# Kernel optimization log

Measured on AMD Instinct MI355X. Metric: run time of the kernel, lower is better.

Reference implementation:

```python
import jax, jax.numpy as jnp
import numpy as np

EMB = 1024
HEAD = 128

def setup_inputs() -> dict:
    key = jax.random.key(0)
    ks = jax.random.split(key, 7)
    B, S = 4, 4096
    x = jax.random.normal(ks[0], (B, S, EMB), dtype=jnp.float32)
    s_in = 1.0 / np.sqrt(EMB)
    Wq = jax.random.uniform(ks[1], (EMB, HEAD), jnp.float32, -s_in, s_in)
    bq = jax.random.uniform(ks[2], (HEAD,), jnp.float32, -s_in, s_in)
    Wk = jax.random.uniform(ks[3], (EMB, HEAD), jnp.float32, -s_in, s_in)
    bk = jax.random.uniform(ks[4], (HEAD,), jnp.float32, -s_in, s_in)
    Wv = jax.random.uniform(ks[5], (EMB, HEAD), jnp.float32, -s_in, s_in)
    bv = jax.random.uniform(ks[6], (HEAD,), jnp.float32, -s_in, s_in)
    return {"decoder_sequence": x, "Wq": Wq, "bq": bq, "Wk": Wk, "bk": bk, "Wv": Wv, "bv": bv}

def reference(decoder_sequence, Wq, bq, Wk, bk, Wv, bv):
    # QKV projections: [B,S,E] @ [E,H] -> [B,S,H]
    Q = decoder_sequence @ Wq + bq
    K = decoder_sequence @ Wk + bk
    V = decoder_sequence @ Wv + bv
    S = decoder_sequence.shape[1]
    scale = 1.0 / jnp.sqrt(jnp.asarray(HEAD, Q.dtype))
    # scores [B,S,S]
    A = jnp.einsum('bid,bjd->bij', Q, K) * scale
    causal = jnp.tril(jnp.ones((S, S), dtype=bool))  # keep lower-triangular incl. diag
    A = jnp.where(causal, A, -jnp.inf)
    A = jax.nn.softmax(A, axis=-1)
    return jnp.einsum('bij,bjd->bid', A, V)
```

## Files before the change

kernel.cpp:

```cpp
#include <hip/hip_runtime.h>
#include <hip/hip_bf16.h>
#include <math.h>

#define S_LEN 4096
#define EMB   1024
#define HEAD  128

typedef short bf16x8 __attribute__((ext_vector_type(8)));
typedef short s16x4  __attribute__((ext_vector_type(4)));
typedef float f32x4  __attribute__((ext_vector_type(4)));
typedef unsigned u32x2 __attribute__((ext_vector_type(2)));
typedef unsigned u32x4 __attribute__((ext_vector_type(4)));

static __device__ __forceinline__ short f2bf(float x){
  unsigned u = __builtin_bit_cast(unsigned, x);
  u += 0x7fffu + ((u >> 16) & 1u);
  return (short)(u >> 16);
}
static __device__ __forceinline__ float bf2f(short s){
  unsigned u = ((unsigned)(unsigned short)s) << 16;
  return __builtin_bit_cast(float, u);
}
static __device__ __forceinline__ unsigned cvtpk(float a, float b){
  unsigned r;
  asm("v_cvt_pk_bf16_f32 %0, %1, %2" : "=v"(r) : "v"(a), "v"(b));
  return r;
}
static __device__ __forceinline__ f32x4 mfma16(bf16x8 a, bf16x8 b, f32x4 c){
  return __builtin_amdgcn_mfma_f32_16x16x32_bf16(a, b, c, 0, 0, 0);
}
static __device__ __forceinline__ void gload16(const void* g, void* l){
  __builtin_amdgcn_global_load_lds((const __attribute__((address_space(1))) unsigned*)g,
                                   (__attribute__((address_space(3))) unsigned*)l, 16, 0, 0);
}

__global__ void prep_w(const float* __restrict__ Wq, const float* __restrict__ bq,
                       const float* __restrict__ Wk, const float* __restrict__ bk,
                       const float* __restrict__ Wv, const float* __restrict__ bv,
                       short* __restrict__ WT, float* __restrict__ bias){
  const float QS = 0.08838834764831845f * 1.4426950408889634f;
  int idx = blockIdx.x * 256 + threadIdx.x;
  int nc  = idx >> 10;
  int k   = idx & 1023;
  int mat = nc >> 7;
  int n   = nc & 127;
  const float* W = (mat == 0) ? Wq : (mat == 1) ? Wk : Wv;
  float s = (mat == 0) ? QS : 1.0f;
  WT[idx] = f2bf(W[k * HEAD + n] * s);
  if (idx < 384){
    int m2 = idx >> 7, n2 = idx & 127;
    const float* bsrc = (m2 == 0) ? bq : (m2 == 1) ? bk : bv;
    float s2 = (m2 == 0) ? QS : 1.0f;
    bias[idx] = bsrc[n2] * s2;
  }
}

__global__ __launch_bounds__(1024) void qkv_proj(const float* __restrict__ x,
    const short* __restrict__ WT, const float* __restrict__ bias,
    short* __restrict__ Qo, short* __restrict__ Ko, short* __restrict__ VTo){
  __shared__ __align__(16) short Sm[2][32768];

  const int tid = threadIdx.x;
  const int wave = tid >> 6, lane = tid & 63, lr = lane & 15, hg = lane >> 4;
  const int wrg = wave >> 3, cg = wave & 7, fbase = cg * 3;
  const int row0 = blockIdx.x * 64;

  const f32x4 zero = {0.f, 0.f, 0.f, 0.f};
  f32x4 acc[2][3];
  #pragma unroll
  for (int rf = 0; rf < 2; ++rf)
    #pragma unroll
    for (int f = 0; f < 3; ++f) acc[rf][f] = zero;

#define WL(buf) (&Sm[buf][0])
#define XL(buf) ((float*)&Sm[buf][24576])

#define QKV_STAGE(buf, k0)                                                         \
  {                                                                                \
    _Pragma("unroll")                                                              \
    for (int s = 0; s < 3; ++s){                                                   \
      int slot = s * 16 + wave;                                                    \
      int ff = slot >> 1, ks = slot & 1;                                           \
      gload16(WT + (size_t)(ff * 16 + lr) * 1024 + (k0) + ks * 32 + hg * 8,        \
              WL(buf) + slot * 512);                                               \
    }                                                                              \
    {                                                                              \
      int rr = wave * 4 + hg;                                                      \
      int cs = lr ^ (rr & 15);                                                     \
      gload16(x + (size_t)(row0 + rr) * 1024 + (k0) + cs * 4,                      \
              XL(buf) + wave * 256);                                               \
    }                                                                              \
  }

  QKV_STAGE(0, 0)

  int cur = 0;
  for (int t = 0; t < 16; ++t){
    if (t < 15){
      QKV_STAGE(cur ^ 1, (t + 1) * 64)
      asm volatile("s_waitcnt vmcnt(4)" ::: "memory");
    } else {
      asm volatile("s_waitcnt vmcnt(0)" ::: "memory");
    }
    __builtin_amdgcn_s_barrier();
    asm volatile("" ::: "memory");

    bf16x8 a[2][2];
    #pragma unroll
    for (int rf = 0; rf < 2; ++rf){
      const int xr = wrg * 32 + rf * 16 + lr;
      #pragma unroll
      for (int ks = 0; ks < 2; ++ks){
        int s0 = ks * 8 + hg * 2;
        f32x4 xa = *(const f32x4*)&XL(cur)[xr * 64 + ((s0 ^ lr) << 2)];
        f32x4 xb = *(const f32x4*)&XL(cur)[xr * 64 + (((s0 + 1) ^ lr) << 2)];
        u32x4 pk = { cvtpk(xa[0], xa[1]), cvtpk(xa[2], xa[3]),
                     cvtpk(xb[0], xb[1]), cvtpk(xb[2], xb[3]) };
        a[rf][ks] = __builtin_bit_cast(bf16x8, pk);
      }
    }
    __builtin_amdgcn_s_setprio(1);
    #pragma unroll
    for (int fi = 0; fi < 3; ++fi){
      #pragma unroll
      for (int ks = 0; ks < 2; ++ks){
        bf16x8 bfr = *(const bf16x8*)&WL(cur)[((fbase + fi) * 2 + ks) * 512 + lane * 8];
        acc[0][fi] = mfma16(a[0][ks], bfr, acc[0][fi]);
        acc[1][fi] = mfma16(a[1][ks], bfr, acc[1][fi]);
      }
    }
    __builtin_amdgcn_s_setprio(0);
    asm volatile("" ::: "memory");
    __builtin_amdgcn_s_barrier();
    cur ^= 1;
  }

  short* Vb = &Sm[0][0];
  #pragma unroll
  for (int rf = 0; rf < 2; ++rf){
    #pragma unroll
    for (int fi = 0; fi < 3; ++fi){
      int f = fbase + fi;
      float bb = bias[f * 16 + lr];
      int rloc = wrg * 32 + rf * 16 + hg * 4;
      u32x2 pk = { cvtpk(acc[rf][fi][0] + bb, acc[rf][fi][1] + bb),
                   cvtpk(acc[rf][fi][2] + bb, acc[rf][fi][3] + bb) };
      s16x4 ov = __builtin_bit_cast(s16x4, pk);
      if (f < 16){
        short* dst = (f < 8) ? Qo : Ko;
        int col = (f & 7) * 16 + lr;
        #pragma unroll
        for (int r = 0; r < 4; ++r)
          dst[(size_t)(row0 + rloc + r) * HEAD + col] = ov[r];
      } else {
        int vcol = (f - 16) * 16 + lr;
        #pragma unroll
        for (int r = 0; r < 4; ++r)
          Vb[vcol * 72 + rloc + r] = ov[r];
      }
    }
  }
  __syncthreads();
  {
    int vcol = tid >> 3, sq = tid & 7;
    bf16x8 v = *(const bf16x8*)&Vb[vcol * 72 + sq * 8];
    int bb2 = row0 >> 12, ss = row0 & 4095;
    *(bf16x8*)(VTo + ((size_t)(bb2 * HEAD + vcol)) * S_LEN + ss + sq * 8) = v;
  }
}

#define PPS 36

__global__ __launch_bounds__(256) void attn(const short* __restrict__ Q,
    const short* __restrict__ K, const short* __restrict__ VT,
    short* __restrict__ Opart, float* __restrict__ Dn){
  __shared__ __align__(16) short Kl[2][4096];
  __shared__ __align__(16) short Vl[2][4096];
  __shared__ __align__(16) short Pl[4][2][16 * PPS];

  const int tid = threadIdx.x;
  const int wave = tid >> 6, lane = tid & 63, lr = lane & 15, hg = lane >> 4;
  const int b = blockIdx.x;
  const int i = blockIdx.y;

  int t, c, ns;
  if (i < 120){
    int acc2 = 0; t = 0; c = 0;
    #pragma unroll
    for (int tt = 0; tt < 32; ++tt){
      int nf = (tt >> 2) + ((tt & 3) == 3);
      if (i >= acc2 && i < acc2 + nf){ t = tt; c = i - acc2; }
      acc2 += nf;
    }
    ns = 16;
  } else if (i < 128){ int k = i - 120; t = 4 * k + 2; c = k; ns = 12; }
  else if (i < 136)  { int k = i - 128; t = 4 * k + 1; c = k; ns = 8; }
  else               { int k = i - 136; t = 4 * k;     c = k; ns = 4; }

  const int qt0  = t * 128;
  const int kvlo = c << 9;

  const short* Qg = Q  + ((size_t)b * S_LEN + qt0 + wave * 32) * HEAD;
  const short* Kg = K  + (size_t)b * S_LEN * HEAD;
  const short* Vg = VT + (size_t)b * HEAD * S_LEN;

  bf16x8 qf[2][4];
  #pragma unroll
  for (int qs = 0; qs < 2; ++qs)
    #pragma unroll
    for (int sl = 0; sl < 4; ++sl)
      qf[qs][sl] = *(const bf16x8*)(Qg + (size_t)(qs * 16 + lr) * HEAD + sl * 32 + hg * 8);

#define ATTN_STAGE(buf, j0)                                                        \
  {                                                                                \
    _Pragma("unroll")                                                              \
    for (int q = 0; q < 2; ++q){                                                   \
      int s = wave * 2 + q;                                                        \
      gload16(Kg + (size_t)((j0) + (s >> 2) * 16 + lr) * HEAD + (s & 3) * 32 + hg * 8, \
              &Kl[buf][s * 512]);                                                  \
    }                                                                              \
    _Pragma("unroll")                                                              \
    for (int q = 0; q < 2; ++q){                                                   \
      int s = wave * 2 + q;                                                        \
      gload16(Vg + (size_t)(s * 16 + lr) * S_LEN + (j0) + hg * 8,                  \
              &Vl[buf][s * 512]);                                                  \
    }                                                                              \
  }

  ATTN_STAGE(0, kvlo)

  const f32x4 zero = {0.f, 0.f, 0.f, 0.f};
  f32x4 acc[8][2];
  #pragma unroll
  for (int f = 0; f < 8; ++f){ acc[f][0] = zero; acc[f][1] = zero; }
  float den[2] = {0.f, 0.f};

  int cur = 0;
  for (int st = 0; st < ns; ++st){
    const int j0 = kvlo + st * 32;
    if (st + 1 < ns){
      ATTN_STAGE(cur ^ 1, j0 + 32)
      asm volatile("s_waitcnt vmcnt(4)" ::: "memory");
    } else {
      asm volatile("s_waitcnt vmcnt(0)" ::: "memory");
    }
    __builtin_amdgcn_s_barrier();
    asm volatile("" ::: "memory");

    f32x4 sc[2][2];
    __builtin_amdgcn_s_setprio(1);
    #pragma unroll
    for (int kvs = 0; kvs < 2; ++kvs){
      sc[kvs][0] = zero; sc[kvs][1] = zero;
      #pragma unroll
      for (int sl = 0; sl < 4; ++sl){
        bf16x8 kf = *(const bf16x8*)&Kl[cur][(kvs * 4 + sl) * 512 + lane * 8];
        sc[kvs][0] = mfma16(kf, qf[0][sl], sc[kvs][0]);
        sc[kvs][1] = mfma16(kf, qf[1][sl], sc[kvs][1]);
      }
    }
    __builtin_amdgcn_s_setprio(0);

    if (j0 + 31 > qt0 + wave * 32){
      #pragma unroll
      for (int qs = 0; qs < 2; ++qs){
        int qr0 = qt0 + wave * 32 + qs * 16;
        #pragma unroll
        for (int kvs = 0; kvs < 2; ++kvs){
          int kv0 = j0 + kvs * 16 + hg * 4;
          #pragma unroll
          for (int r = 0; r < 4; ++r)
            if (kv0 + r > qr0 + lr) sc[kvs][qs][r] = -INFINITY;
        }
      }
    }

    s16x4 pb[2][2];
    #pragma unroll
    for (int qs = 0; qs < 2; ++qs){
      float p0[4], p1[4];
      #pragma unroll
      for (int r = 0; r < 4; ++r){
        p0[r] = __builtin_exp2f(sc[0][qs][r]);
        p1[r] = __builtin_exp2f(sc[1][qs][r]);
        den[qs] += p0[r] + p1[r];
      }
      u32x2 w0 = { cvtpk(p0[0], p0[1]), cvtpk(p0[2], p0[3]) };
      u32x2 w1 = { cvtpk(p1[0], p1[1]), cvtpk(p1[2], p1[3]) };
      pb[qs][0] = __builtin_bit_cast(s16x4, w0);
      pb[qs][1] = __builtin_bit_cast(s16x4, w1);
    }

    #pragma unroll
    for (int qs = 0; qs < 2; ++qs){
      short* Pw = &Pl[wave][qs][0];
      *(s16x4*)(&Pw[lr * PPS + hg * 4])      = pb[qs][0];
      *(s16x4*)(&Pw[lr * PPS + 16 + hg * 4]) = pb[qs][1];
    }
    bf16x8 vf[8];
    #pragma unroll
    for (int f = 0; f < 8; ++f)
      vf[f] = *(const bf16x8*)&Vl[cur][f * 512 + lane * 8];
    bf16x8 pf[2];
    #pragma unroll
    for (int qs = 0; qs < 2; ++qs)
      pf[qs] = *(const bf16x8*)(&Pl[wave][qs][lr * PPS + hg * 8]);

    __builtin_amdgcn_s_setprio(1);
    #pragma unroll
    for (int f = 0; f < 8; ++f){
      acc[f][0] = mfma16(vf[f], pf[0], acc[f][0]);
      acc[f][1] = mfma16(vf[f], pf[1], acc[f][1]);
    }
    __builtin_amdgcn_s_setprio(0);

    asm volatile("" ::: "memory");
    __builtin_amdgcn_s_barrier();
    cur ^= 1;
  }

  #pragma unroll
  for (int qs = 0; qs < 2; ++qs){
    den[qs] += __shfl_xor(den[qs], 16);
    den[qs] += __shfl_xor(den[qs], 32);
  }

  const int pidx = b * 144 + i;
  short* Op = Opart + (size_t)pidx * 16384;
  #pragma unroll
  for (int qs = 0; qs < 2; ++qs){
    const int rowblk = wave * 2 + qs;
    #pragma unroll
    for (int f = 0; f < 8; ++f){
      u32x2 pk = { cvtpk(acc[f][qs][0], acc[f][qs][1]),
                   cvtpk(acc[f][qs][2], acc[f][qs][3]) };
      *(u32x2*)(Op + (rowblk * 16 + lr) * 128 + f * 16 + hg * 4) = pk;
    }
    if (hg == 0)
      Dn[pidx * 128 + rowblk * 16 + lr] = den[qs];
  }
}

__global__ __launch_bounds__(512) void combine(const short* __restrict__ Opart,
    const float* __restrict__ Dn, float* __restrict__ out){
  const int bx = blockIdx.x, b = blockIdx.y;
  const int t = bx >> 1, sub = bx & 1;
  const int row = threadIdx.x >> 3;
  const int cgp = threadIdx.x & 7;
  const int rI = sub * 64 + row;
  const int a = t >> 2, bb = t & 3;
  const int Ffull = a * (2 * a + bb - 1);
  const int nfull = a + (bb == 3);
  const int nc = a + 1;
  const int ipart = (bb == 2) ? 120 + a : (bb == 1) ? 128 + a : 136 + a;

  float L = 0.f;
  float o[16];
  #pragma unroll
  for (int e = 0; e < 16; ++e) o[e] = 0.f;
  for (int cc = 0; cc < nc; ++cc){
    int ii = (cc < nfull) ? Ffull + cc : ipart;
    int id = b * 144 + ii;
    L += Dn[id * 128 + rI];
    const short* op = Opart + (size_t)id * 16384 + rI * 128 + cgp * 16;
    bf16x8 v0 = *(const bf16x8*)(op);
    bf16x8 v1 = *(const bf16x8*)(op + 8);
    #pragma unroll
    for (int e = 0; e < 8; ++e){
      o[e]     += bf2f(v0[e]);
      o[8 + e] += bf2f(v1[e]);
    }
  }
  float inv = 1.f / L;
  float* dst = out + ((size_t)b * S_LEN + t * 128 + rI) * HEAD + cgp * 16;
  #pragma unroll
  for (int e4 = 0; e4 < 4; ++e4){
    float4 w4 = { o[e4*4]*inv, o[e4*4+1]*inv, o[e4*4+2]*inv, o[e4*4+3]*inv };
    *(float4*)(dst + e4 * 4) = w4;
  }
}

extern "C" void kernel_launch(void* const* d_in, const int* in_sizes, int n_in,
                              void* d_out, int out_size, void* d_ws, size_t ws_size,
                              hipStream_t stream){
  const float* x  = (const float*)d_in[0];
  const float* Wq = (const float*)d_in[1];
  const float* bq = (const float*)d_in[2];
  const float* Wk = (const float*)d_in[3];
  const float* bk = (const float*)d_in[4];
  const float* Wv = (const float*)d_in[5];
  const float* bv = (const float*)d_in[6];
  float* out = (float*)d_out;

  char* ws = (char*)d_ws;
  short* WT    = (short*)(ws);
  float* bias  = (float*)(ws + 786432);
  short* Qb    = (short*)(ws + (1u << 20));
  short* Kb    = (short*)(ws + (1u << 20) + 4194304u);
  short* VTb   = (short*)(ws + (1u << 20) + 8388608u);
  short* Opart = (short*)(ws + 13631488u);
  float* Dn    = (float*)(ws + 32505856u);

  prep_w<<<1536, 256, 0, stream>>>(Wq, bq, Wk, bk, Wv, bv, WT, bias);
  qkv_proj<<<256, 1024, 0, stream>>>(x, WT, bias, Qb, Kb, VTb);
  attn<<<dim3(4, 144), 256, 0, stream>>>(Qb, Kb, VTb, Opart, Dn);
  combine<<<dim3(64, 4), 512, 0, stream>>>(Opart, Dn, out);
}
```

Measured before the change: 89.83 us.

## Software-pipeline PV MFMA one stage behind QK with triple-buffered V

Defers the P·V matrix multiply of each KV stage into the next iteration, placing it right after the QK^T MFMAs so it can overlap the softmax/exp and P store of the current stage. V shared buffers grow from two to three so the previous stage's V tile stays resident while the next one is prefetched, and a final epilogue drains the last PV step. This adds LDS usage (an extra 8KB) and carries the P fragments across iterations in registers, which may lower occupancy or raise register pressure.

```diff
diff --git a/kernel.cpp b/kernel.cpp
--- a/kernel.cpp
+++ b/kernel.cpp
@@ -175,7 +175,7 @@
     const short* __restrict__ K, const short* __restrict__ VT,
     short* __restrict__ Opart, float* __restrict__ Dn){
   __shared__ __align__(16) short Kl[2][4096];
-  __shared__ __align__(16) short Vl[2][4096];
+  __shared__ __align__(16) short Vl[3][4096];
   __shared__ __align__(16) short Pl[4][2][16 * PPS];
 
   const int tid = threadIdx.x;
@@ -211,35 +211,38 @@
     for (int sl = 0; sl < 4; ++sl)
       qf[qs][sl] = *(const bf16x8*)(Qg + (size_t)(qs * 16 + lr) * HEAD + sl * 32 + hg * 8);
 
-#define ATTN_STAGE(buf, j0)                                                        \
+#define ATTN_STAGE(kb, vb, j0)                                                     \
   {                                                                                \
     _Pragma("unroll")                                                              \
     for (int q = 0; q < 2; ++q){                                                   \
       int s = wave * 2 + q;                                                        \
       gload16(Kg + (size_t)((j0) + (s >> 2) * 16 + lr) * HEAD + (s & 3) * 32 + hg * 8, \
-              &Kl[buf][s * 512]);                                                  \
+              &Kl[kb][s * 512]);                                                   \
     }                                                                              \
     _Pragma("unroll")                                                              \
     for (int q = 0; q < 2; ++q){                                                   \
       int s = wave * 2 + q;                                                        \
       gload16(Vg + (size_t)(s * 16 + lr) * S_LEN + (j0) + hg * 8,                  \
-              &Vl[buf][s * 512]);                                                  \
+              &Vl[vb][s * 512]);                                                   \
     }                                                                              \
   }
 
-  ATTN_STAGE(0, kvlo)
+  ATTN_STAGE(0, 0, kvlo)
 
   const f32x4 zero = {0.f, 0.f, 0.f, 0.f};
   f32x4 acc[8][2];
   #pragma unroll
   for (int f = 0; f < 8; ++f){ acc[f][0] = zero; acc[f][1] = zero; }
   float den[2] = {0.f, 0.f};
-
-  int cur = 0;
+  bf16x8 pfp[2];
+
+  int kc = 0, vcur = 0;
   for (int st = 0; st < ns; ++st){
     const int j0 = kvlo + st * 32;
+    const int vnxt = (vcur + 1 == 3) ? 0 : vcur + 1;
+    const int vprv = (vcur == 0) ? 2 : vcur - 1;
     if (st + 1 < ns){
-      ATTN_STAGE(cur ^ 1, j0 + 32)
+      ATTN_STAGE(kc ^ 1, vnxt, j0 + 32)
       asm volatile("s_waitcnt vmcnt(4)" ::: "memory");
     } else {
       asm volatile("s_waitcnt vmcnt(0)" ::: "memory");
@@ -254,12 +257,23 @@
       sc[kvs][0] = zero; sc[kvs][1] = zero;
       #pragma unroll
       for (int sl = 0; sl < 4; ++sl){
-        bf16x8 kf = *(const bf16x8*)&Kl[cur][(kvs * 4 + sl) * 512 + lane * 8];
+        bf16x8 kf = *(const bf16x8*)&Kl[kc][(kvs * 4 + sl) * 512 + lane * 8];
         sc[kvs][0] = mfma16(kf, qf[0][sl], sc[kvs][0]);
         sc[kvs][1] = mfma16(kf, qf[1][sl], sc[kvs][1]);
       }
     }
     __builtin_amdgcn_s_setprio(0);
+
+    if (st > 0){
+      __builtin_amdgcn_s_setprio(1);
+      #pragma unroll
+      for (int f = 0; f < 8; ++f){
+        bf16x8 vf = *(const bf16x8*)&Vl[vprv][f * 512 + lane * 8];
+        acc[f][0] = mfma16(vf, pfp[0], acc[f][0]);
+        acc[f][1] = mfma16(vf, pfp[1], acc[f][1]);
+      }
+      __builtin_amdgcn_s_setprio(0);
+    }
 
     if (j0 + 31 > qt0 + wave * 32){
       #pragma unroll
@@ -297,26 +311,23 @@
       *(s16x4*)(&Pw[lr * PPS + hg * 4])      = pb[qs][0];
       *(s16x4*)(&Pw[lr * PPS + 16 + hg * 4]) = pb[qs][1];
     }
-    bf16x8 vf[8];
-    #pragma unroll
-    for (int f = 0; f < 8; ++f)
-      vf[f] = *(const bf16x8*)&Vl[cur][f * 512 + lane * 8];
-    bf16x8 pf[2];
     #pragma unroll
     for (int qs = 0; qs < 2; ++qs)
-      pf[qs] = *(const bf16x8*)(&Pl[wave][qs][lr * PPS + hg * 8]);
-
-    __builtin_amdgcn_s_setprio(1);
-    #pragma unroll
-    for (int f = 0; f < 8; ++f){
-      acc[f][0] = mfma16(vf[f], pf[0], acc[f][0]);
-      acc[f][1] = mfma16(vf[f], pf[1], acc[f][1]);
-    }
-    __builtin_amdgcn_s_setprio(0);
+      pfp[qs] = *(const bf16x8*)(&Pl[wave][qs][lr * PPS + hg * 8]);
 
     asm volatile("" ::: "memory");
     __builtin_amdgcn_s_barrier();
-    cur ^= 1;
+    kc ^= 1; vcur = vnxt;
+  }
+
+  {
+    const int vprv = (vcur == 0) ? 2 : vcur - 1;
+    #pragma unroll
+    for (int f = 0; f < 8; ++f){
+      bf16x8 vf = *(const bf16x8*)&Vl[vprv][f * 512 + lane * 8];
+      acc[f][0] = mfma16(vf, pfp[0], acc[f][0]);
+      acc[f][1] = mfma16(vf, pfp[1], acc[f][1]);
+    }
   }
 
   #pragma unroll
```

New measurement: 89.69 us. About the same (-0.2%).
